# Kernel optimization log

Hardware: AMD Instinct MI355X
Metric: run time of the kernel (lower is better)

Reference implementation:

```python
import jax, jax.numpy as jnp
import numpy as np

G, NPG, D_IN, HID, NH, DH = 128, 256, 15, 128, 8, 16
N = G * NPG
E = 1_048_576
NLAYERS = 3
EPS = 1e-5


def ln(x, g, b):
    m = x.mean(-1, keepdims=True)
    v = ((x - m) ** 2).mean(-1, keepdims=True)
    return (x - m) * jax.lax.rsqrt(v + EPS) * g + b


def gcn_conv(x, src, dst, W, b):
    # PyG GCNConv: add self-loops, symmetric deg^-1/2 normalization
    n = x.shape[0]
    h = x @ W  # [N, H]
    loop = jnp.arange(n)
    s = jnp.concatenate([src, loop])
    d = jnp.concatenate([dst, loop])
    deg = jnp.zeros((n,), x.dtype).at[d].add(1.0)  # >=1 due to self-loops
    dis = jax.lax.rsqrt(deg)
    coef = (dis[s] * dis[d])[:, None]
    return jnp.zeros_like(h).at[d].add(h[s] * coef) + b


def setup_inputs() -> dict:
    key = jax.random.key(0)
    ks = jax.random.split(key, 40)
    i = iter(range(40))

    def w(shape, scale=0.05):
        return jax.random.normal(ks[next(i)], shape, jnp.float32) * scale

    inp = {
        'x': jax.random.normal(ks[next(i)], (N, D_IN), jnp.float32),
        'edge_index': jax.random.randint(ks[next(i)], (2, E), 0, N),
        'batch': jnp.repeat(jnp.arange(G), NPG),  # 128 graphs x 256 nodes
        # input_proj: Linear + LayerNorm
        'W_in': w((D_IN, HID)), 'b_in': jnp.zeros((HID,)),
        'g_in': jnp.ones((HID,)), 'be_in': jnp.zeros((HID,)),
        # 3 GCNConv layers + LayerNorms (stacked)
        'Wc': w((NLAYERS, HID, HID)), 'bc': jnp.zeros((NLAYERS, HID)),
        'gn': jnp.ones((NLAYERS, HID)), 'bn': jnp.zeros((NLAYERS, HID)),
        # MultiheadAttention (in_proj split into q/k/v) + out_proj + post-LN
        'Wq': w((HID, HID)), 'bq': jnp.zeros((HID,)),
        'Wk': w((HID, HID)), 'bk': jnp.zeros((HID,)),
        'Wv': w((HID, HID)), 'bv': jnp.zeros((HID,)),
        'Wo': w((HID, HID)), 'bo': jnp.zeros((HID,)),
        'ga': jnp.ones((HID,)), 'ba': jnp.zeros((HID,)),
        # classifier: Linear(3H->H)+LN, Linear(H->H//2), Linear(H//2->2)
        'W1': w((3 * HID, HID)), 'b1': jnp.zeros((HID,)),
        'g1': jnp.ones((HID,)), 'beta1': jnp.zeros((HID,)),
        'W2': w((HID, HID // 2)), 'b2': jnp.zeros((HID // 2,)),
        'W3': w((HID // 2, 2)), 'b3': jnp.zeros((2,)),
    }
    return inp


def reference(x, edge_index, batch, W_in, b_in, g_in, be_in, Wc, bc, gn, bn,
              Wq, bq, Wk, bk, Wv, bv, Wo, bo, ga, ba,
              W1, b1, g1, beta1, W2, b2, W3, b3):
    src, dst = edge_index[0], edge_index[1]
    # input_proj (dropout is identity in eval)
    h = jax.nn.relu(ln(x @ W_in + b_in, g_in, be_in))
    # causal_graph_forward: GCN + LN + ReLU, residual for layers > 0
    for i in range(NLAYERS):
        h_res = h
        h = jax.nn.relu(ln(gcn_conv(h, src, dst, Wc[i], bc[i]), gn[i], bn[i]))
        if i > 0:
            h = h + h_res
    # per-graph MHA: equal-sized graphs -> block-diagonal == batched attention
    hg = h.reshape(G, NPG, HID)
    scale = 1.0 / np.sqrt(DH).astype(np.float32)
    q = (hg @ Wq.T + bq).reshape(G, NPG, NH, DH).transpose(0, 2, 1, 3)
    k = (hg @ Wk.T + bk).reshape(G, NPG, NH, DH).transpose(0, 2, 1, 3)
    v = (hg @ Wv.T + bv).reshape(G, NPG, NH, DH).transpose(0, 2, 1, 3)
    att = jax.nn.softmax(jnp.einsum('ghid,ghjd->ghij', q, k) * scale, axis=-1)
    o = jnp.einsum('ghij,ghjd->ghid', att, v).transpose(0, 2, 1, 3).reshape(G, NPG, HID)
    hg = ln(o @ Wo.T + bo + hg, ga, ba)
    # global mean/max/sum pooling per graph
    pooled = jnp.concatenate([hg.mean(1), hg.max(1), hg.sum(1)], axis=-1)  # [G, 3H]
    # classifier
    z = jax.nn.relu(ln(pooled @ W1 + b1, g1, beta1))
    z = jax.nn.relu(z @ W2 + b2)
    return z @ W3 + b3
```

## Files before the change

### kernel.cpp

```cpp
#include <hip/hip_runtime.h>
#include <hip/hip_bf16.h>

#define N_NODES 32768
#define E_EDGES 1048576
#define HID 128
#define G_GRAPHS 128
#define NPG 256
#define NH 8
#define DH 16
#define EPS 1e-5f
#define CHUNK 4096
#define BCAP 8192

typedef __attribute__((ext_vector_type(4))) float f32x4;
typedef __attribute__((ext_vector_type(4))) short bf16x4;

static __device__ __forceinline__ unsigned short bfbits(float f) {
    return __builtin_bit_cast(unsigned short, __float2bfloat16(f));
}
static __device__ __forceinline__ float bf2f(unsigned short u) {
    return __builtin_bit_cast(float, (unsigned)u << 16);
}

__device__ __forceinline__ void ln_stats128(float v, float& mean, float& istd, float* red) {
    float s = v, s2 = v * v;
#pragma unroll
    for (int off = 32; off; off >>= 1) { s += __shfl_xor(s, off); s2 += __shfl_xor(s2, off); }
    int w = threadIdx.x >> 6;
    if ((threadIdx.x & 63) == 0) { red[w * 2] = s; red[w * 2 + 1] = s2; }
    __syncthreads();
    float ts = red[0] + red[2], ts2 = red[1] + red[3];
    mean = ts * (1.f / 128.f);
    float var = ts2 * (1.f / 128.f) - mean * mean;
    istd = rsqrtf(var + EPS);
    __syncthreads();
}

__global__ __launch_bounds__(256) void bucket_count(const int* __restrict__ dst,
                                                    int* __restrict__ bucket_cnt) {
    __shared__ int bcnt[256];
    int tid = threadIdx.x;
    bcnt[tid] = 0;
    __syncthreads();
    int base = blockIdx.x * CHUNK;
#pragma unroll
    for (int j = 0; j < 16; j++) {
        int d = dst[base + j * 256 + tid];
        atomicAdd(&bcnt[d >> 7], 1);
    }
    __syncthreads();
    atomicAdd(&bucket_cnt[tid], bcnt[tid]);
}

__global__ __launch_bounds__(256) void scan_buckets(const int* __restrict__ bucket_cnt,
                                                    int* __restrict__ bucket_base,
                                                    int* __restrict__ bucket_fill) {
    __shared__ int sc[256];
    int t = threadIdx.x;
    int c = bucket_cnt[t];
    sc[t] = c;
    __syncthreads();
    for (int off = 1; off < 256; off <<= 1) {
        int v = (t >= off) ? sc[t - off] : 0;
        __syncthreads();
        sc[t] += v;
        __syncthreads();
    }
    int ex = sc[t] - c;
    bucket_base[t] = ex;
    bucket_fill[t] = ex;
    if (t == 255) bucket_base[256] = sc[255];
}

__global__ __launch_bounds__(256) void bucket_scatter(const int* __restrict__ src,
                                                      const int* __restrict__ dst,
                                                      int* __restrict__ bucket_fill,
                                                      int* __restrict__ packed) {
    __shared__ int bcnt[256];
    __shared__ int lsc[256];
    __shared__ int delta[256];
    __shared__ int sorted[CHUNK];
    int tid = threadIdx.x;
    int base = blockIdx.x * CHUNK;
    int pk[16], bk[16], rk[16];
    bcnt[tid] = 0;
    __syncthreads();
#pragma unroll
    for (int j = 0; j < 16; j++) {
        int e = base + j * 256 + tid;
        int d = dst[e], s = src[e];
        pk[j] = (d << 15) | s;
        bk[j] = d >> 7;
    }
#pragma unroll
    for (int j = 0; j < 16; j++) rk[j] = atomicAdd(&bcnt[bk[j]], 1);
    __syncthreads();
    int cnt_t = bcnt[tid];
    lsc[tid] = cnt_t;
    __syncthreads();
    for (int off = 1; off < 256; off <<= 1) {
        int v = (tid >= off) ? lsc[tid - off] : 0;
        __syncthreads();
        lsc[tid] += v;
        __syncthreads();
    }
    int ls_t = lsc[tid] - cnt_t;
    __syncthreads();
    lsc[tid] = ls_t;
    int g = 0;
    if (cnt_t > 0) g = atomicAdd(&bucket_fill[tid], cnt_t);
    delta[tid] = g - ls_t;
    __syncthreads();
#pragma unroll
    for (int j = 0; j < 16; j++) sorted[lsc[bk[j]] + rk[j]] = pk[j];
    __syncthreads();
    for (int i = tid; i < CHUNK; i += 256) {
        int u = sorted[i];
        int b2 = u >> 22;
        packed[delta[b2] + i] = u;
    }
}

__global__ __launch_bounds__(256) void csr_build(const int* __restrict__ bucket_base,
                                                 const int* __restrict__ packed,
                                                 int* __restrict__ srcs,
                                                 int* __restrict__ row_ptr,
                                                 float* __restrict__ dis) {
    __shared__ int ncnt[128];
    __shared__ int sc[128];
    __shared__ int fill[128];
    __shared__ int outl[BCAP];
    int b = blockIdx.x, tid = threadIdx.x;
    int c0 = bucket_base[b], c1 = bucket_base[b + 1];
    int cnt = c1 - c0;
    if (tid < 128) ncnt[tid] = 0;
    __syncthreads();
    for (int i = tid; i < cnt; i += 256) {
        int u = packed[c0 + i];
        atomicAdd(&ncnt[(u >> 15) & 127], 1);
    }
    __syncthreads();
    int c = (tid < 128) ? ncnt[tid] : 0;
    if (tid < 128) sc[tid] = c;
    __syncthreads();
    for (int off = 1; off < 128; off <<= 1) {
        int v = (tid < 128 && tid >= off) ? sc[tid - off] : 0;
        __syncthreads();
        if (tid < 128) sc[tid] += v;
        __syncthreads();
    }
    if (tid < 128) {
        int ex = sc[tid] - c;
        fill[tid] = ex;
        int node = b * 128 + tid;
        row_ptr[node] = c0 + ex;
        dis[node] = rsqrtf((float)(c + 1));
    }
    if (b == 255 && tid == 0) row_ptr[N_NODES] = c1;
    __syncthreads();
    if (cnt <= BCAP) {
        for (int i = tid; i < cnt; i += 256) {
            int u = packed[c0 + i];
            int p = atomicAdd(&fill[(u >> 15) & 127], 1);
            outl[p] = u & 32767;
        }
        __syncthreads();
        for (int i = tid; i < cnt; i += 256) srcs[c0 + i] = outl[i];
    } else {
        for (int i = tid; i < cnt; i += 256) {
            int u = packed[c0 + i];
            int p = atomicAdd(&fill[(u >> 15) & 127], 1);
            srcs[c0 + p] = u & 32767;
        }
    }
}

__global__ __launch_bounds__(256) void prep_weights(const float* __restrict__ Wc,
                                                    const float* __restrict__ Wq,
                                                    const float* __restrict__ Wk,
                                                    const float* __restrict__ Wv,
                                                    const float* __restrict__ Wo,
                                                    const float* __restrict__ bq,
                                                    const float* __restrict__ bk,
                                                    const float* __restrict__ bv,
                                                    unsigned short* __restrict__ Wpk,
                                                    float* __restrict__ bT) {
    int m = blockIdx.y;
    int idx = blockIdx.x * 256 + threadIdx.x;
    int j = idx & 3, ln = (idx >> 2) & 63, kt = (idx >> 8) & 7, jt = (idx >> 11) & 7;
    int k = kt * 16 + (ln >> 4) * 4 + j;
    int col = jt * 16 + (ln & 15);
    float val;
    if (m < 3) val = Wc[m * 16384 + k * 128 + col];
    else {
        const float* W = (m == 3) ? Wq : (m == 4) ? Wk : (m == 5) ? Wv : Wo;
        val = W[col * 128 + k];
    }
    Wpk[m * 16384 + idx] = bfbits(val);
    if (m >= 3 && m < 6 && idx < 128) {
        const float* bs = (m == 3) ? bq : (m == 4) ? bk : bv;
        bT[(m - 3) * 128 + idx] = bs[idx];
    }
}

__global__ __launch_bounds__(128) void input_proj(const float* __restrict__ x,
                                                  const float* __restrict__ W,
                                                  const float* __restrict__ b,
                                                  const float* __restrict__ g,
                                                  const float* __restrict__ be,
                                                  unsigned short* __restrict__ h16) {
    int n = blockIdx.x, j = threadIdx.x;
    __shared__ float xs[15];
    __shared__ float red[4];
    if (j < 15) xs[j] = x[n * 15 + j];
    __syncthreads();
    float acc = b[j];
#pragma unroll
    for (int k = 0; k < 15; k++) acc += xs[k] * W[k * 128 + j];
    float m, is;
    ln_stats128(acc, m, is, red);
    float y = (acc - m) * is * g[j] + be[j];
    h16[(long)n * 128 + j] = bfbits(fmaxf(y, 0.f));
}

template <int MODE>
__device__ __forceinline__ void gemm_mfma_body(const unsigned short* __restrict__ in16,
                                               const unsigned short* __restrict__ Wpk,
                                               const float* __restrict__ bias,
                                               const unsigned short* __restrict__ resid16,
                                               const float* __restrict__ gamma,
                                               const float* __restrict__ beta,
                                               unsigned short* __restrict__ out16) {
    __shared__ unsigned short Ws[16384];
    __shared__ unsigned short Hs[64][136];
    int tid = threadIdx.x;
    long base = (long)blockIdx.x * 64;
    {
        const uint4* s4 = (const uint4*)Wpk;
        uint4* d4 = (uint4*)Ws;
        for (int i = tid; i < 2048; i += 256) d4[i] = s4[i];
        const unsigned short* hsrc = in16 + base * 128;
        for (int i = tid; i < 1024; i += 256) {
            int r = i >> 4, c8 = i & 15;
            *(uint4*)&Hs[r][c8 * 8] = *(const uint4*)&hsrc[r * 128 + c8 * 8];
        }
    }
    __syncthreads();
    int wv = tid >> 6, lane = tid & 63;
    int ql = lane & 15, qg = lane >> 4;
    f32x4 acc[8];
#pragma unroll
    for (int jt = 0; jt < 8; jt++) acc[jt] = (f32x4){0.f, 0.f, 0.f, 0.f};
#pragma unroll
    for (int kt = 0; kt < 8; kt++) {
        bf16x4 af = *(const bf16x4*)&Hs[wv * 16 + ql][kt * 16 + qg * 4];
#pragma unroll
        for (int jt = 0; jt < 8; jt++) {
            bf16x4 bf = *(const bf16x4*)&Ws[((jt * 8 + kt) * 64 + lane) * 4];
            acc[jt] = __builtin_amdgcn_mfma_f32_16x16x16bf16_1k(af, bf, acc[jt], 0, 0, 0);
        }
    }
    if (MODE >= 1) {
#pragma unroll
        for (int jt = 0; jt < 8; jt++) {
            float bv = bias[jt * 16 + ql];
#pragma unroll
            for (int r = 0; r < 4; r++) acc[jt][r] += bv;
        }
    }
    if (MODE == 2) {
#pragma unroll
        for (int jt = 0; jt < 8; jt++)
#pragma unroll
            for (int r = 0; r < 4; r++)
                acc[jt][r] += bf2f(resid16[(base + wv * 16 + qg * 4 + r) * 128 + jt * 16 + ql]);
        float s[4], s2[4], mean[4], istd[4];
#pragma unroll
        for (int r = 0; r < 4; r++) { s[r] = 0.f; s2[r] = 0.f; }
#pragma unroll
        for (int jt = 0; jt < 8; jt++)
#pragma unroll
            for (int r = 0; r < 4; r++) { float v = acc[jt][r]; s[r] += v; s2[r] += v * v; }
#pragma unroll
        for (int off = 1; off < 16; off <<= 1)
#pragma unroll
            for (int r = 0; r < 4; r++) {
                s[r] += __shfl_xor(s[r], off);
                s2[r] += __shfl_xor(s2[r], off);
            }
#pragma unroll
        for (int r = 0; r < 4; r++) {
            mean[r] = s[r] * (1.f / 128.f);
            float var = s2[r] * (1.f / 128.f) - mean[r] * mean[r];
            istd[r] = rsqrtf(var + EPS);
        }
#pragma unroll
        for (int jt = 0; jt < 8; jt++) {
            float gv = gamma[jt * 16 + ql], bev = beta[jt * 16 + ql];
#pragma unroll
            for (int r = 0; r < 4; r++)
                acc[jt][r] = (acc[jt][r] - mean[r]) * istd[r] * gv + bev;
        }
    }
#pragma unroll
    for (int jt = 0; jt < 8; jt++)
#pragma unroll
        for (int r = 0; r < 4; r++)
            Hs[wv * 16 + qg * 4 + r][jt * 16 + ql] = bfbits(acc[jt][r]);
#pragma unroll
    for (int p = 0; p < 4; p++) {
        int rl = p * 4 + qg;
        uint4 v = *(const uint4*)&Hs[wv * 16 + rl][ql * 8];
        *(uint4*)&out16[(base + wv * 16 + rl) * 128 + ql * 8] = v;
    }
}

template <int MODE>
__global__ __launch_bounds__(256) void gemm_mfma(const unsigned short* __restrict__ in16,
                                                 const unsigned short* __restrict__ Wpk,
                                                 const float* __restrict__ bias,
                                                 const unsigned short* __restrict__ resid16,
                                                 const float* __restrict__ gamma,
                                                 const float* __restrict__ beta,
                                                 unsigned short* __restrict__ out16) {
    gemm_mfma_body<MODE>(in16, Wpk, bias, resid16, gamma, beta, out16);
}

__global__ __launch_bounds__(256) void gemm_qkv(const unsigned short* __restrict__ in16,
                                                const unsigned short* __restrict__ Wpk,
                                                const float* __restrict__ bT,
                                                unsigned short* __restrict__ outb) {
    int y = blockIdx.y;
    gemm_mfma_body<1>(in16, Wpk + (3 + y) * 16384, bT + y * 128, nullptr, nullptr, nullptr,
                      outb + (long)y * N_NODES * 128);
}

__global__ __launch_bounds__(256) void gcn_agg(const unsigned short* __restrict__ hW,
                                               const int* __restrict__ row_ptr,
                                               const int* __restrict__ srcs,
                                               const float* __restrict__ dis,
                                               const float* __restrict__ bias,
                                               const float* __restrict__ gamma,
                                               const float* __restrict__ beta,
                                               unsigned short* __restrict__ h16, int with_resid) {
    int wv = threadIdx.x >> 6, lane = threadIdx.x & 63;
    int n = blockIdx.x * 4 + wv;
    int r0 = row_ptr[n], r1 = row_ptr[n + 1];
    float dn = dis[n];
    unsigned su = *(const unsigned*)&hW[(long)n * 128 + lane * 2];
    float dnn = dn * dn;
    float a0 = bf2f((unsigned short)(su & 0xffff)) * dnn;
    float a1 = bf2f((unsigned short)(su >> 16)) * dnn;
    for (int b = r0; b < r1; b += 64) {
        int cnt = min(64, r1 - b);
        int sv = n;
        float cv = 0.f;
        if (lane < cnt) {
            sv = srcs[b + lane];
            cv = dis[sv] * dn;
        }
        int cntR = (cnt + 15) & ~15;
        for (int j = 0; j < cntR; j += 16) {
            unsigned u[16];
#pragma unroll
            for (int t = 0; t < 16; t++) {
                int s = __builtin_amdgcn_readlane(sv, j + t);
                u[t] = *(const unsigned*)&hW[(long)s * 128 + lane * 2];
            }
#pragma unroll
            for (int t = 0; t < 16; t++) {
                float c = __builtin_bit_cast(float,
                            __builtin_amdgcn_readlane(__builtin_bit_cast(int, cv), j + t));
                a0 += bf2f((unsigned short)(u[t] & 0xffff)) * c;
                a1 += bf2f((unsigned short)(u[t] >> 16)) * c;
            }
        }
    }
    float2 bb = *(const float2*)&bias[lane * 2];
    a0 += bb.x;
    a1 += bb.y;
    float s = a0 + a1, s2 = a0 * a0 + a1 * a1;
#pragma unroll
    for (int off = 1; off < 64; off <<= 1) { s += __shfl_xor(s, off); s2 += __shfl_xor(s2, off); }
    float mean = s * (1.f / 128.f);
    float var = s2 * (1.f / 128.f) - mean * mean;
    float is = rsqrtf(var + EPS);
    float2 gg = *(const float2*)&gamma[lane * 2];
    float2 be2 = *(const float2*)&beta[lane * 2];
    float y0 = fmaxf((a0 - mean) * is * gg.x + be2.x, 0.f);
    float y1 = fmaxf((a1 - mean) * is * gg.y + be2.y, 0.f);
    if (with_resid) {
        unsigned ru = *(const unsigned*)&h16[(long)n * 128 + lane * 2];
        y0 += bf2f((unsigned short)(ru & 0xffff));
        y1 += bf2f((unsigned short)(ru >> 16));
    }
    unsigned outu = (unsigned)bfbits(y0) | ((unsigned)bfbits(y1) << 16);
    *(unsigned*)&h16[(long)n * 128 + lane * 2] = outu;
}

__global__ __launch_bounds__(256) void attention(const unsigned short* __restrict__ q16,
                                                 const unsigned short* __restrict__ k16,
                                                 const unsigned short* __restrict__ v16,
                                                 unsigned short* __restrict__ o16) {
    int g = blockIdx.x, hh = blockIdx.y;
    int tid = threadIdx.x;
    long gbase = ((long)g * NPG) * 128 + hh * 16;
    __shared__ unsigned short Ksh[256][24];
    __shared__ unsigned short Qsh[256][24];
    __shared__ unsigned short Vt[16][264];
    {
        const unsigned short* kp = k16 + gbase + (long)tid * 128;
        uint4 a = *(const uint4*)kp, b = *(const uint4*)(kp + 8);
        *(uint4*)&Ksh[tid][0] = a; *(uint4*)&Ksh[tid][8] = b;
        const unsigned short* qp = q16 + gbase + (long)tid * 128;
        uint4 c = *(const uint4*)qp, d = *(const uint4*)(qp + 8);
        *(uint4*)&Qsh[tid][0] = c; *(uint4*)&Qsh[tid][8] = d;
        const unsigned short* vp = v16 + gbase + (long)tid * 128;
#pragma unroll
        for (int dd = 0; dd < 16; dd++) Vt[dd][tid] = vp[dd];
    }
    __syncthreads();
    int wv = tid >> 6, lane = tid & 63;
    int qg = lane >> 4, ql = lane & 15;
    bf16x4 vfrag[16];
#pragma unroll
    for (int kt = 0; kt < 16; kt++)
        vfrag[kt] = *(const bf16x4*)&Vt[ql][kt * 16 + qg * 4];
    const float C = 0.36067376022224085f;
    for (int qi = 0; qi < 4; qi++) {
        int qt = wv * 4 + qi;
        bf16x4 qfrag = *(const bf16x4*)&Qsh[qt * 16 + ql][qg * 4];
        float lsum = 0.f;
        bf16x4 pb[16];
        f32x4 z4 = {0.f, 0.f, 0.f, 0.f};
#pragma unroll
        for (int kt = 0; kt < 16; kt++) {
            bf16x4 kfrag = *(const bf16x4*)&Ksh[kt * 16 + ql][qg * 4];
            f32x4 s4 = __builtin_amdgcn_mfma_f32_16x16x16bf16_1k(kfrag, qfrag, z4, 0, 0, 0);
            bf16x4 pbk;
#pragma unroll
            for (int r = 0; r < 4; r++) {
                float pv = exp2f(s4[r] * C);
                lsum += pv;
                pbk[r] = (short)bfbits(pv);
            }
            pb[kt] = pbk;
        }
        f32x4 oacc = {0.f, 0.f, 0.f, 0.f};
#pragma unroll
        for (int kt = 0; kt < 16; kt++)
            oacc = __builtin_amdgcn_mfma_f32_16x16x16bf16_1k(vfrag[kt], pb[kt], oacc, 0, 0, 0);
        lsum += __shfl_xor(lsum, 16);
        lsum += __shfl_xor(lsum, 32);
        float inv = 1.f / lsum;
        unsigned short* op = o16 + gbase + (long)(qt * 16 + ql) * 128 + 4 * qg;
        ushort4 st;
        st.x = bfbits(oacc[0] * inv);
        st.y = bfbits(oacc[1] * inv);
        st.z = bfbits(oacc[2] * inv);
        st.w = bfbits(oacc[3] * inv);
        *(ushort4*)op = st;
    }
}

__global__ __launch_bounds__(256) void pool_kernel(const unsigned short* __restrict__ hg,
                                                   float* __restrict__ pooled) {
    int g = blockIdx.x;
    int lane = threadIdx.x & 63, grp = threadIdx.x >> 6;
    __shared__ float ssum[4][128];
    __shared__ float smax[4][128];
    float s0 = 0.f, s1 = 0.f, m0 = -1e30f, m1 = -1e30f;
    for (int i = grp * 64; i < grp * 64 + 64; i++) {
        unsigned u = *(const unsigned*)&hg[((long)g * NPG + i) * 128 + lane * 2];
        float v0 = bf2f((unsigned short)(u & 0xffff));
        float v1 = bf2f((unsigned short)(u >> 16));
        s0 += v0; s1 += v1;
        m0 = fmaxf(m0, v0); m1 = fmaxf(m1, v1);
    }
    ssum[grp][lane * 2] = s0; ssum[grp][lane * 2 + 1] = s1;
    smax[grp][lane * 2] = m0; smax[grp][lane * 2 + 1] = m1;
    __syncthreads();
    if (grp == 0) {
        for (int jj = lane; jj < 128; jj += 64) {
            float ts = ssum[0][jj] + ssum[1][jj] + ssum[2][jj] + ssum[3][jj];
            float tm = fmaxf(fmaxf(smax[0][jj], smax[1][jj]), fmaxf(smax[2][jj], smax[3][jj]));
            pooled[g * 384 + jj] = ts * (1.f / 256.f);
            pooled[g * 384 + 128 + jj] = tm;
            pooled[g * 384 + 256 + jj] = ts;
        }
    }
}

__global__ __launch_bounds__(128) void classifier(const float* __restrict__ pooled,
                                                  const float* __restrict__ W1, const float* __restrict__ b1,
                                                  const float* __restrict__ g1, const float* __restrict__ be1,
                                                  const float* __restrict__ W2, const float* __restrict__ b2,
                                                  const float* __restrict__ W3, const float* __restrict__ b3,
                                                  float* __restrict__ out) {
    int g = blockIdx.x, j = threadIdx.x;
    __shared__ float pl[384];
    __shared__ float z1s[128];
    __shared__ float z2s[64];
    __shared__ float red[4];
    for (int i = j; i < 384; i += 128) pl[i] = pooled[g * 384 + i];
    __syncthreads();
    float acc = b1[j];
    for (int kk = 0; kk < 384; kk++) acc += pl[kk] * W1[kk * 128 + j];
    float m, is;
    ln_stats128(acc, m, is, red);
    float y = fmaxf((acc - m) * is * g1[j] + be1[j], 0.f);
    z1s[j] = y;
    __syncthreads();
    if (j < 64) {
        float a2 = b2[j];
        for (int kk = 0; kk < 128; kk++) a2 += z1s[kk] * W2[kk * 64 + j];
        z2s[j] = fmaxf(a2, 0.f);
    }
    __syncthreads();
    if (j < 64) {
        float vv = z2s[j];
        float p0 = vv * W3[j * 2];
        float p1 = vv * W3[j * 2 + 1];
#pragma unroll
        for (int off = 32; off; off >>= 1) { p0 += __shfl_xor(p0, off); p1 += __shfl_xor(p1, off); }
        if (j == 0) {
            out[g * 2] = p0 + b3[0];
            out[g * 2 + 1] = p1 + b3[1];
        }
    }
}

extern "C" void kernel_launch(void* const* d_in, const int* in_sizes, int n_in,
                              void* d_out, int out_size, void* d_ws, size_t ws_size,
                              hipStream_t stream) {
    const float* x = (const float*)d_in[0];
    const int* ei = (const int*)d_in[1];
    const float* W_in = (const float*)d_in[3];
    const float* b_in = (const float*)d_in[4];
    const float* g_in = (const float*)d_in[5];
    const float* be_in = (const float*)d_in[6];
    const float* Wc = (const float*)d_in[7];
    const float* bc = (const float*)d_in[8];
    const float* gn = (const float*)d_in[9];
    const float* bn = (const float*)d_in[10];
    const float* Wq = (const float*)d_in[11];
    const float* bq = (const float*)d_in[12];
    const float* Wk = (const float*)d_in[13];
    const float* bk = (const float*)d_in[14];
    const float* Wv = (const float*)d_in[15];
    const float* bv = (const float*)d_in[16];
    const float* Wo = (const float*)d_in[17];
    const float* bo = (const float*)d_in[18];
    const float* ga = (const float*)d_in[19];
    const float* ba = (const float*)d_in[20];
    const float* W1 = (const float*)d_in[21];
    const float* b1 = (const float*)d_in[22];
    const float* g1 = (const float*)d_in[23];
    const float* be1 = (const float*)d_in[24];
    const float* W2 = (const float*)d_in[25];
    const float* b2 = (const float*)d_in[26];
    const float* W3 = (const float*)d_in[27];
    const float* b3 = (const float*)d_in[28];
    float* out = (float*)d_out;

    const long NF = (long)N_NODES * 128;
    unsigned char* wsb = (unsigned char*)d_ws;
    const size_t MB = 1 << 20;
    unsigned short* h16 = (unsigned short*)(wsb);
    unsigned short* hw16 = (unsigned short*)(wsb + 8 * MB);
    unsigned short* qkv16 = (unsigned short*)(wsb + 16 * MB);
    unsigned short* o16 = (unsigned short*)(wsb + 40 * MB);
    unsigned short* hg16 = (unsigned short*)(wsb + 48 * MB);
    unsigned short* Wpk = (unsigned short*)(wsb + 56 * MB);
    int* packed = (int*)(wsb + 57 * MB);
    int* srcs = (int*)(wsb + 61 * MB);
    int* row_ptr = (int*)(wsb + 65 * MB);
    float* dis = (float*)(wsb + 66 * MB);
    float* bT = (float*)(wsb + 67 * MB);
    float* pooled = (float*)(wsb + 67 * MB + 4096);
    int* bucket_cnt = (int*)(wsb + 68 * MB);
    int* bucket_base = bucket_cnt + 256;
    int* bucket_fill = bucket_base + 257;

    const int* e_src = ei;
    const int* e_dst = ei + E_EDGES;

    hipMemsetAsync(bucket_cnt, 0, 256 * sizeof(int), stream);
    prep_weights<<<dim3(64, 7), 256, 0, stream>>>(Wc, Wq, Wk, Wv, Wo, bq, bk, bv, Wpk, bT);
    bucket_count<<<E_EDGES / CHUNK, 256, 0, stream>>>(e_dst, bucket_cnt);
    scan_buckets<<<1, 256, 0, stream>>>(bucket_cnt, bucket_base, bucket_fill);
    bucket_scatter<<<E_EDGES / CHUNK, 256, 0, stream>>>(e_src, e_dst, bucket_fill, packed);
    csr_build<<<256, 256, 0, stream>>>(bucket_base, packed, srcs, row_ptr, dis);

    input_proj<<<N_NODES, 128, 0, stream>>>(x, W_in, b_in, g_in, be_in, h16);

    for (int i = 0; i < 3; i++) {
        gemm_mfma<0><<<N_NODES / 64, 256, 0, stream>>>(h16, Wpk + i * 16384, nullptr, nullptr,
                                                       nullptr, nullptr, hw16);
        gcn_agg<<<N_NODES / 4, 256, 0, stream>>>(hw16, row_ptr, srcs, dis, bc + i * 128,
                                                 gn + i * 128, bn + i * 128, h16, i > 0);
    }

    gemm_qkv<<<dim3(N_NODES / 64, 3), 256, 0, stream>>>(h16, Wpk, bT, qkv16);

    attention<<<dim3(G_GRAPHS, NH), 256, 0, stream>>>(qkv16, qkv16 + NF, qkv16 + 2 * NF, o16);

    gemm_mfma<2><<<N_NODES / 64, 256, 0, stream>>>(o16, Wpk + 6 * 16384, bo, h16, ga, ba, hg16);

    pool_kernel<<<G_GRAPHS, 256, 0, stream>>>(hg16, pooled);
    classifier<<<G_GRAPHS, 128, 0, stream>>>(pooled, W1, b1, g1, be1, W2, b2, W3, b3, out);
}
```

Measured before the change: 365.2 us.

## Split gcn_agg wave into two half-wave edge streams, rework input_proj, fuse pool+classifier

gcn_agg now has each half-wave handle a different edge, with each lane loading 8 bytes (4 bf16 features) instead of 4. The two halves' partial sums are combined by a cross-half shuffle before the LayerNorm. input_proj now processes one node per wave with 4 nodes per block, replacing one 128-thread block per node and removing shared memory and syncs. Pooling and the classifier are merged into one kernel that splits the W1 matvec across 256 threads, saving a launch and the global round-trip for pooled. The risk is extra readlane/select overhead per edge pair and some wasted lanes when a node has an odd edge count.

```diff
diff --git a/kernel.cpp b/kernel.cpp
--- a/kernel.cpp
+++ b/kernel.cpp
@@ -21,6 +21,9 @@
 static __device__ __forceinline__ float bf2f(unsigned short u) {
     return __builtin_bit_cast(float, (unsigned)u << 16);
 }
+static __device__ __forceinline__ float rdlanef(float v, int l) {
+    return __builtin_bit_cast(float, __builtin_amdgcn_readlane(__builtin_bit_cast(int, v), l));
+}
 
 __device__ __forceinline__ void ln_stats128(float v, float& mean, float& istd, float* red) {
     float s = v, s2 = v * v;
@@ -30,6 +33,21 @@
     if ((threadIdx.x & 63) == 0) { red[w * 2] = s; red[w * 2 + 1] = s2; }
     __syncthreads();
     float ts = red[0] + red[2], ts2 = red[1] + red[3];
+    mean = ts * (1.f / 128.f);
+    float var = ts2 * (1.f / 128.f) - mean * mean;
+    istd = rsqrtf(var + EPS);
+    __syncthreads();
+}
+
+__device__ __forceinline__ void ln_stats256(float v, float& mean, float& istd, float* red8) {
+    float s = v, s2 = v * v;
+#pragma unroll
+    for (int off = 32; off; off >>= 1) { s += __shfl_xor(s, off); s2 += __shfl_xor(s2, off); }
+    int w = threadIdx.x >> 6;
+    if ((threadIdx.x & 63) == 0) { red8[w * 2] = s; red8[w * 2 + 1] = s2; }
+    __syncthreads();
+    float ts = red8[0] + red8[2] + red8[4] + red8[6];
+    float ts2 = red8[1] + red8[3] + red8[5] + red8[7];
     mean = ts * (1.f / 128.f);
     float var = ts2 * (1.f / 128.f) - mean * mean;
     istd = rsqrtf(var + EPS);
@@ -203,24 +221,37 @@
     }
 }
 
-__global__ __launch_bounds__(128) void input_proj(const float* __restrict__ x,
+__global__ __launch_bounds__(256) void input_proj(const float* __restrict__ x,
                                                   const float* __restrict__ W,
                                                   const float* __restrict__ b,
                                                   const float* __restrict__ g,
                                                   const float* __restrict__ be,
                                                   unsigned short* __restrict__ h16) {
-    int n = blockIdx.x, j = threadIdx.x;
-    __shared__ float xs[15];
-    __shared__ float red[4];
-    if (j < 15) xs[j] = x[n * 15 + j];
-    __syncthreads();
-    float acc = b[j];
-#pragma unroll
-    for (int k = 0; k < 15; k++) acc += xs[k] * W[k * 128 + j];
-    float m, is;
-    ln_stats128(acc, m, is, red);
-    float y = (acc - m) * is * g[j] + be[j];
-    h16[(long)n * 128 + j] = bfbits(fmaxf(y, 0.f));
+    int wv = threadIdx.x >> 6, lane = threadIdx.x & 63;
+    int n = blockIdx.x * 4 + wv;
+    float xv = (lane < 15) ? x[n * 15 + lane] : 0.f;
+    int c = lane * 2;
+    float2 bb = *(const float2*)&b[c];
+    float a0 = bb.x, a1 = bb.y;
+#pragma unroll
+    for (int k = 0; k < 15; k++) {
+        float xk = rdlanef(xv, k);
+        float2 w2 = *(const float2*)&W[k * 128 + c];
+        a0 += xk * w2.x;
+        a1 += xk * w2.y;
+    }
+    float s = a0 + a1, s2 = a0 * a0 + a1 * a1;
+#pragma unroll
+    for (int off = 1; off < 64; off <<= 1) { s += __shfl_xor(s, off); s2 += __shfl_xor(s2, off); }
+    float mean = s * (1.f / 128.f);
+    float var = s2 * (1.f / 128.f) - mean * mean;
+    float is = rsqrtf(var + EPS);
+    float2 gg = *(const float2*)&g[c];
+    float2 be2 = *(const float2*)&be[c];
+    float y0 = fmaxf((a0 - mean) * is * gg.x + be2.x, 0.f);
+    float y1 = fmaxf((a1 - mean) * is * gg.y + be2.y, 0.f);
+    unsigned outu = (unsigned)bfbits(y0) | ((unsigned)bfbits(y1) << 16);
+    *(unsigned*)&h16[(long)n * 128 + c] = outu;
 }
 
 template <int MODE>
@@ -347,10 +378,17 @@
     int n = blockIdx.x * 4 + wv;
     int r0 = row_ptr[n], r1 = row_ptr[n + 1];
     float dn = dis[n];
-    unsigned su = *(const unsigned*)&hW[(long)n * 128 + lane * 2];
-    float dnn = dn * dn;
-    float a0 = bf2f((unsigned short)(su & 0xffff)) * dnn;
-    float a1 = bf2f((unsigned short)(su >> 16)) * dnn;
+    int l32 = lane & 31;
+    int hi = lane >> 5;
+    float a0, a1, a2, a3;
+    {
+        uint2 su = *(const uint2*)&hW[(long)n * 128 + l32 * 4];
+        float dh = dn * dn * 0.5f;
+        a0 = bf2f((unsigned short)(su.x & 0xffff)) * dh;
+        a1 = bf2f((unsigned short)(su.x >> 16)) * dh;
+        a2 = bf2f((unsigned short)(su.y & 0xffff)) * dh;
+        a3 = bf2f((unsigned short)(su.y >> 16)) * dh;
+    }
     for (int b = r0; b < r1; b += 64) {
         int cnt = min(64, r1 - b);
         int sv = n;
@@ -359,43 +397,63 @@
             sv = srcs[b + lane];
             cv = dis[sv] * dn;
         }
-        int cntR = (cnt + 15) & ~15;
-        for (int j = 0; j < cntR; j += 16) {
-            unsigned u[16];
-#pragma unroll
-            for (int t = 0; t < 16; t++) {
-                int s = __builtin_amdgcn_readlane(sv, j + t);
-                u[t] = *(const unsigned*)&hW[(long)s * 128 + lane * 2];
+        int pairs = (cnt + 1) >> 1;
+        int pR = (pairs + 7) & ~7;
+        for (int j = 0; j < pR; j += 8) {
+            uint2 u[8];
+#pragma unroll
+            for (int t = 0; t < 8; t++) {
+                int e0 = 2 * (j + t);
+                int s0 = __builtin_amdgcn_readlane(sv, e0);
+                int s1 = __builtin_amdgcn_readlane(sv, e0 + 1);
+                int ss = hi ? s1 : s0;
+                u[t] = *(const uint2*)&hW[(long)ss * 128 + l32 * 4];
             }
 #pragma unroll
-            for (int t = 0; t < 16; t++) {
-                float c = __builtin_bit_cast(float,
-                            __builtin_amdgcn_readlane(__builtin_bit_cast(int, cv), j + t));
-                a0 += bf2f((unsigned short)(u[t] & 0xffff)) * c;
-                a1 += bf2f((unsigned short)(u[t] >> 16)) * c;
+            for (int t = 0; t < 8; t++) {
+                int e0 = 2 * (j + t);
+                float c0 = rdlanef(cv, e0);
+                float c1 = rdlanef(cv, e0 + 1);
+                float c = hi ? c1 : c0;
+                a0 += bf2f((unsigned short)(u[t].x & 0xffff)) * c;
+                a1 += bf2f((unsigned short)(u[t].x >> 16)) * c;
+                a2 += bf2f((unsigned short)(u[t].y & 0xffff)) * c;
+                a3 += bf2f((unsigned short)(u[t].y >> 16)) * c;
             }
         }
     }
-    float2 bb = *(const float2*)&bias[lane * 2];
-    a0 += bb.x;
-    a1 += bb.y;
-    float s = a0 + a1, s2 = a0 * a0 + a1 * a1;
-#pragma unroll
-    for (int off = 1; off < 64; off <<= 1) { s += __shfl_xor(s, off); s2 += __shfl_xor(s2, off); }
+    a0 += __shfl_xor(a0, 32);
+    a1 += __shfl_xor(a1, 32);
+    a2 += __shfl_xor(a2, 32);
+    a3 += __shfl_xor(a3, 32);
+    float4 bb = *(const float4*)&bias[l32 * 4];
+    a0 += bb.x; a1 += bb.y; a2 += bb.z; a3 += bb.w;
+    float s = a0 + a1 + a2 + a3;
+    float s2 = a0 * a0 + a1 * a1 + a2 * a2 + a3 * a3;
+#pragma unroll
+    for (int off = 1; off < 32; off <<= 1) { s += __shfl_xor(s, off); s2 += __shfl_xor(s2, off); }
     float mean = s * (1.f / 128.f);
     float var = s2 * (1.f / 128.f) - mean * mean;
     float is = rsqrtf(var + EPS);
-    float2 gg = *(const float2*)&gamma[lane * 2];
-    float2 be2 = *(const float2*)&beta[lane * 2];
-    float y0 = fmaxf((a0 - mean) * is * gg.x + be2.x, 0.f);
-    float y1 = fmaxf((a1 - mean) * is * gg.y + be2.y, 0.f);
+    float4 gg = *(const float4*)&gamma[l32 * 4];
+    float4 be4 = *(const float4*)&beta[l32 * 4];
+    float y0 = fmaxf((a0 - mean) * is * gg.x + be4.x, 0.f);
+    float y1 = fmaxf((a1 - mean) * is * gg.y + be4.y, 0.f);
+    float y2 = fmaxf((a2 - mean) * is * gg.z + be4.z, 0.f);
+    float y3 = fmaxf((a3 - mean) * is * gg.w + be4.w, 0.f);
     if (with_resid) {
-        unsigned ru = *(const unsigned*)&h16[(long)n * 128 + lane * 2];
-        y0 += bf2f((unsigned short)(ru & 0xffff));
-        y1 += bf2f((unsigned short)(ru >> 16));
-    }
-    unsigned outu = (unsigned)bfbits(y0) | ((unsigned)bfbits(y1) << 16);
-    *(unsigned*)&h16[(long)n * 128 + lane * 2] = outu;
+        uint2 ru = *(const uint2*)&h16[(long)n * 128 + l32 * 4];
+        y0 += bf2f((unsigned short)(ru.x & 0xffff));
+        y1 += bf2f((unsigned short)(ru.x >> 16));
+        y2 += bf2f((unsigned short)(ru.y & 0xffff));
+        y3 += bf2f((unsigned short)(ru.y >> 16));
+    }
+    if (hi == 0) {
+        uint2 outu;
+        outu.x = (unsigned)bfbits(y0) | ((unsigned)bfbits(y1) << 16);
+        outu.y = (unsigned)bfbits(y2) | ((unsigned)bfbits(y3) << 16);
+        *(uint2*)&h16[(long)n * 128 + l32 * 4] = outu;
+    }
 }
 
 __global__ __launch_bounds__(256) void attention(const unsigned short* __restrict__ q16,
@@ -463,12 +521,22 @@
     }
 }
 
-__global__ __launch_bounds__(256) void pool_kernel(const unsigned short* __restrict__ hg,
-                                                   float* __restrict__ pooled) {
+__global__ __launch_bounds__(256) void pool_classifier(const unsigned short* __restrict__ hg,
+                                                       const float* __restrict__ W1, const float* __restrict__ b1,
+                                                       const float* __restrict__ g1, const float* __restrict__ be1,
+                                                       const float* __restrict__ W2, const float* __restrict__ b2,
+                                                       const float* __restrict__ W3, const float* __restrict__ b3,
+                                                       float* __restrict__ out) {
     int g = blockIdx.x;
-    int lane = threadIdx.x & 63, grp = threadIdx.x >> 6;
+    int tid = threadIdx.x;
+    int lane = tid & 63, grp = tid >> 6;
     __shared__ float ssum[4][128];
     __shared__ float smax[4][128];
+    __shared__ float pl[384];
+    __shared__ float zpart[2][128];
+    __shared__ float z1s[128];
+    __shared__ float z2s[64];
+    __shared__ float red8[8];
     float s0 = 0.f, s1 = 0.f, m0 = -1e30f, m1 = -1e30f;
     for (int i = grp * 64; i < grp * 64 + 64; i++) {
         unsigned u = *(const unsigned*)&hg[((long)g * NPG + i) * 128 + lane * 2];
@@ -480,50 +548,41 @@
     ssum[grp][lane * 2] = s0; ssum[grp][lane * 2 + 1] = s1;
     smax[grp][lane * 2] = m0; smax[grp][lane * 2 + 1] = m1;
     __syncthreads();
-    if (grp == 0) {
-        for (int jj = lane; jj < 128; jj += 64) {
-            float ts = ssum[0][jj] + ssum[1][jj] + ssum[2][jj] + ssum[3][jj];
-            float tm = fmaxf(fmaxf(smax[0][jj], smax[1][jj]), fmaxf(smax[2][jj], smax[3][jj]));
-            pooled[g * 384 + jj] = ts * (1.f / 256.f);
-            pooled[g * 384 + 128 + jj] = tm;
-            pooled[g * 384 + 256 + jj] = ts;
-        }
-    }
-}
-
-__global__ __launch_bounds__(128) void classifier(const float* __restrict__ pooled,
-                                                  const float* __restrict__ W1, const float* __restrict__ b1,
-                                                  const float* __restrict__ g1, const float* __restrict__ be1,
-                                                  const float* __restrict__ W2, const float* __restrict__ b2,
-                                                  const float* __restrict__ W3, const float* __restrict__ b3,
-                                                  float* __restrict__ out) {
-    int g = blockIdx.x, j = threadIdx.x;
-    __shared__ float pl[384];
-    __shared__ float z1s[128];
-    __shared__ float z2s[64];
-    __shared__ float red[4];
-    for (int i = j; i < 384; i += 128) pl[i] = pooled[g * 384 + i];
-    __syncthreads();
-    float acc = b1[j];
-    for (int kk = 0; kk < 384; kk++) acc += pl[kk] * W1[kk * 128 + j];
+    if (tid < 128) {
+        float ts = ssum[0][tid] + ssum[1][tid] + ssum[2][tid] + ssum[3][tid];
+        float tm = fmaxf(fmaxf(smax[0][tid], smax[1][tid]), fmaxf(smax[2][tid], smax[3][tid]));
+        pl[tid] = ts * (1.f / 256.f);
+        pl[128 + tid] = tm;
+        pl[256 + tid] = ts;
+    }
+    __syncthreads();
+    {
+        int j = tid & 127, half = tid >> 7;
+        float part = 0.f;
+        for (int kk = half * 192; kk < half * 192 + 192; kk++)
+            part += pl[kk] * W1[kk * 128 + j];
+        zpart[half][j] = part;
+    }
+    __syncthreads();
+    float acc = 0.f;
+    if (tid < 128) acc = b1[tid] + zpart[0][tid] + zpart[1][tid];
     float m, is;
-    ln_stats128(acc, m, is, red);
-    float y = fmaxf((acc - m) * is * g1[j] + be1[j], 0.f);
-    z1s[j] = y;
-    __syncthreads();
-    if (j < 64) {
-        float a2 = b2[j];
-        for (int kk = 0; kk < 128; kk++) a2 += z1s[kk] * W2[kk * 64 + j];
-        z2s[j] = fmaxf(a2, 0.f);
-    }
-    __syncthreads();
-    if (j < 64) {
-        float vv = z2s[j];
-        float p0 = vv * W3[j * 2];
-        float p1 = vv * W3[j * 2 + 1];
+    ln_stats256(tid < 128 ? acc : 0.f, m, is, red8);
+    if (tid < 128) z1s[tid] = fmaxf((acc - m) * is * g1[tid] + be1[tid], 0.f);
+    __syncthreads();
+    if (tid < 64) {
+        float a2 = b2[tid];
+        for (int kk = 0; kk < 128; kk++) a2 += z1s[kk] * W2[kk * 64 + tid];
+        z2s[tid] = fmaxf(a2, 0.f);
+    }
+    __syncthreads();
+    if (tid < 64) {
+        float vv = z2s[tid];
+        float p0 = vv * W3[tid * 2];
+        float p1 = vv * W3[tid * 2 + 1];
 #pragma unroll
         for (int off = 32; off; off >>= 1) { p0 += __shfl_xor(p0, off); p1 += __shfl_xor(p1, off); }
-        if (j == 0) {
+        if (tid == 0) {
             out[g * 2] = p0 + b3[0];
             out[g * 2 + 1] = p1 + b3[1];
         }
@@ -577,7 +636,6 @@
     int* row_ptr = (int*)(wsb + 65 * MB);
     float* dis = (float*)(wsb + 66 * MB);
     float* bT = (float*)(wsb + 67 * MB);
-    float* pooled = (float*)(wsb + 67 * MB + 4096);
     int* bucket_cnt = (int*)(wsb + 68 * MB);
     int* bucket_base = bucket_cnt + 256;
     int* bucket_fill = bucket_base + 257;
@@ -592,7 +650,7 @@
     bucket_scatter<<<E_EDGES / CHUNK, 256, 0, stream>>>(e_src, e_dst, bucket_fill, packed);
     csr_build<<<256, 256, 0, stream>>>(bucket_base, packed, srcs, row_ptr, dis);
 
-    input_proj<<<N_NODES, 128, 0, stream>>>(x, W_in, b_in, g_in, be_in, h16);
+    input_proj<<<N_NODES / 4, 256, 0, stream>>>(x, W_in, b_in, g_in, be_in, h16);
 
     for (int i = 0; i < 3; i++) {
         gemm_mfma<0><<<N_NODES / 64, 256, 0, stream>>>(h16, Wpk + i * 16384, nullptr, nullptr,
@@ -607,6 +665,5 @@
 
     gemm_mfma<2><<<N_NODES / 64, 256, 0, stream>>>(o16, Wpk + 6 * 16384, bo, h16, ga, ba, hg16);
 
-    pool_kernel<<<G_GRAPHS, 256, 0, stream>>>(hg16, pooled);
-    classifier<<<G_GRAPHS, 128, 0, stream>>>(pooled, W1, b1, g1, be1, W2, b2, W3, b3, out);
-}
+    pool_classifier<<<G_GRAPHS, 256, 0, stream>>>(hg16, W1, b1, g1, be1, W2, b2, W3, b3, out);
+}
```

After: 383.0 us. 4.9% more time.
